# Performance work log

Hardware: AMD Instinct MI355X
Metric: run time of the kernel (lower is better)

The kernel has to match this reference:

```python
import jax, jax.numpy as jnp
import numpy as np

NUM_CODE = 8192
CODE_DIM = 256


def setup_inputs() -> dict:
    key = jax.random.key(0)
    k1, k2 = jax.random.split(key)
    z_e = jax.random.normal(k1, (16, CODE_DIM, 32, 32), dtype=jnp.float32)
    span = 1.0 / NUM_CODE
    codebook = jax.random.uniform(k2, (NUM_CODE, CODE_DIM), dtype=jnp.float32,
                                  minval=-span, maxval=span)
    return {"z_e": z_e, "codebook": codebook}


def reference(z_e, codebook):
    # NCHW -> NHWC
    z = jnp.transpose(z_e, (0, 2, 3, 1))  # [B,H,W,D]
    B, H, W, D = z.shape
    flat = z.reshape(-1, D)  # [N,D]
    cb = jax.lax.stop_gradient(codebook)
    # squared L2 distances without materializing [N,K,D] diff tensor
    z2 = jnp.sum(flat * flat, axis=1, keepdims=True)          # [N,1]
    c2 = jnp.sum(cb * cb, axis=1)                              # [K]
    dist = z2 - 2.0 * (flat @ cb.T) + c2[None, :]              # [N,K]
    indices = jnp.argmin(dist, axis=1)                         # [N]
    z_q_flat = cb[indices]                                     # [N,D]
    z_q = z_q_flat.reshape(B, H, W, D)
    # straight-through estimator
    z_q = z + jax.lax.stop_gradient(z_q - z)
    idx = indices.reshape(B, H, W)
    z_q = jnp.transpose(z_q, (0, 3, 1, 2))  # NHWC -> NCHW
    return z_q, idx
```

## Files before the change

kernel.cpp:

```cpp
#include <hip/hip_runtime.h>

typedef __attribute__((ext_vector_type(4))) unsigned int u32x4;
typedef __attribute__((ext_vector_type(4))) int i32x4;

union I16 { u32x4 u; i32x4 i; };

#define SA_INV   (127.0f / 12.0f)
#define SB_INV   (127.0f * 8192.0f)
#define INV_SASB ((127.0 * 127.0 * 8192.0) / 12.0)
#define WI       4500
#define FINF     3.4e38f

__device__ __forceinline__ int q8(float x, float s) {
    int q = (int)__builtin_rintf(x * s);
    return q < -127 ? -127 : (q > 127 ? 127 : q);
}
__device__ __forceinline__ unsigned int umin(unsigned int a, unsigned int b) { return a < b ? a : b; }
__device__ __forceinline__ unsigned int umax(unsigned int a, unsigned int b) { return a > b ? a : b; }

__global__ __launch_bounds__(256)
void prep_z(const float* __restrict__ z, u32x4* __restrict__ ahi,
            float* __restrict__ zt, float* __restrict__ z2f) {
    __shared__ float tile[32][257];
    __shared__ double pz[32][9];
    int bh = blockIdx.x;
    int b = bh >> 5, h = bh & 31;
    int tid = threadIdx.x;
    for (int e = tid; e < 8192; e += 256) {
        int d = e >> 5, w = e & 31;
        tile[w][d] = z[((size_t)(b * 256 + d) * 32 + h) * 32 + w];
    }
    __syncthreads();
    for (int e = tid; e < 8192; e += 256) {
        int w = e >> 8, d = e & 255;
        zt[(size_t)(bh * 32 + w) * 256 + d] = tile[w][d];
    }
    {
        int w = tid >> 3, seg = tid & 7;
        double s = 0.0;
#pragma unroll
        for (int d = 0; d < 32; ++d) { double v = (double)tile[w][seg * 32 + d]; s += v * v; }
        pz[w][seg] = s;
    }
    __syncthreads();
    if (tid < 32) {
        double s = 0.0;
#pragma unroll
        for (int seg = 0; seg < 8; ++seg) s += pz[tid][seg];
        z2f[bh * 32 + tid] = (float)s;
    }
    for (int o = tid; o < 512; o += 256) {
        int l = o & 63, j = (o >> 6) & 3, tt = o >> 8;
        int wp = tt * 16 + (l & 15);
        int k0 = j * 64 + ((l >> 4) << 4);
        u32x4 v;
#pragma unroll
        for (int d = 0; d < 4; ++d) {
            unsigned int wv = 0;
#pragma unroll
            for (int bb = 0; bb < 4; ++bb) {
                int q = q8(-2.0f * tile[wp][k0 + d * 4 + bb], SA_INV);
                wv |= ((unsigned int)(q & 255)) << (8 * bb);
            }
            v[d] = wv;
        }
        ahi[(size_t)bh * 512 + o] = v;
    }
}

__global__ __launch_bounds__(256)
void prep_cb(const float* __restrict__ cb, float* __restrict__ c2,
             unsigned int* __restrict__ ibt, u32x4* __restrict__ bstr) {
    __shared__ float tile[16][257];
    __shared__ float pc[16][17];
    int ct = blockIdx.x;
    int tid = threadIdx.x;
    int cl = tid >> 4, dseg = tid & 15;
    const float* src = cb + (size_t)(ct * 16 + cl) * 256 + dseg * 16;
    float s = 0.f;
#pragma unroll
    for (int i = 0; i < 16; ++i) { float v = src[i]; tile[cl][dseg * 16 + i] = v; s += v * v; }
    pc[cl][dseg] = s;
    __syncthreads();
    if (tid < 16) {
        float t = 0.f;
#pragma unroll
        for (int i = 0; i < 16; ++i) t += pc[tid][i];
        int code = ct * 16 + tid;
        c2[code] = t;
        int ib = (int)__builtin_rintf(t * (float)INV_SASB);
        ibt[code] = (((unsigned int)(ib + 262144)) << 6) | (unsigned int)((code >> 4) & 31);
    }
    int l = tid & 63, j = tid >> 6;
    int code_l = l & 15, k0 = j * 64 + ((l >> 4) << 4);
    u32x4 v;
#pragma unroll
    for (int d = 0; d < 4; ++d) {
        unsigned int wv = 0;
#pragma unroll
        for (int bb = 0; bb < 4; ++bb) {
            int q = q8(tile[code_l][k0 + d * 4 + bb], SB_INV);
            wv |= ((unsigned int)(q & 255)) << (8 * bb);
        }
        v[d] = wv;
    }
    bstr[(size_t)(ct * 4 + j) * 64 + l] = v;
}

__global__ __launch_bounds__(256)
void vq_main(const u32x4* __restrict__ ahi4, const u32x4* __restrict__ bstr,
             const unsigned int* __restrict__ ibt,
             unsigned int* __restrict__ cd, int* __restrict__ ci) {
    int tid = threadIdx.x;
    int wid = tid >> 6, lane = tid & 63;
    int stripe = blockIdx.x & 15;
    int rg = blockIdx.x >> 4;
    int colc = lane & 15;
    int rt0 = rg * 16 + wid * 4;

    I16 ah[4][4];
#pragma unroll
    for (int rt = 0; rt < 4; ++rt)
#pragma unroll
        for (int j = 0; j < 4; ++j)
            ah[rt][j].u = ahi4[((size_t)(rt0 + rt) * 4 + j) * 64 + lane];

    unsigned int m1[16], m2[16];
#pragma unroll
    for (int s = 0; s < 16; ++s) { m1[s] = 0xFFFFFFFFu; m2[s] = 0xFFFFFFFFu; }

    const u32x4* bbase = bstr + (size_t)stripe * 8192 + lane;
    const unsigned int* ibase = ibt + stripe * 512 + colc;
    i32x4 zc = (i32x4){0, 0, 0, 0};

    I16 bfA[4], bfB[4];
    unsigned int ibA, ibB;
#pragma unroll
    for (int j = 0; j < 4; ++j) bfA[j].u = bbase[j * 64];
    ibA = ibase[0];

    auto tilework = [&](const I16 (&bf)[4], unsigned int ibv) {
        i32x4 acc[4];
#pragma unroll
        for (int rt = 0; rt < 4; ++rt)
            acc[rt] = __builtin_amdgcn_mfma_i32_16x16x64_i8(ah[rt][0].i, bf[0].i, zc, 0, 0, 0);
#pragma unroll
        for (int j = 1; j < 4; ++j)
#pragma unroll
            for (int rt = 0; rt < 4; ++rt)
                acc[rt] = __builtin_amdgcn_mfma_i32_16x16x64_i8(ah[rt][j].i, bf[j].i, acc[rt], 0, 0, 0);
#pragma unroll
        for (int rt = 0; rt < 4; ++rt)
#pragma unroll
            for (int r = 0; r < 4; ++r) {
                unsigned int key = (((unsigned int)acc[rt][r]) << 6) + ibv;
                int s = rt * 4 + r;
                m2[s] = umin(umax(key, m1[s]), m2[s]);
                m1[s] = umin(m1[s], key);
            }
    };

    for (int t = 0; t < 32; t += 2) {
#pragma unroll
        for (int j = 0; j < 4; ++j) bfB[j].u = bbase[(t + 1) * 256 + j * 64];
        ibB = ibase[(t + 1) * 16];
        tilework(bfA, ibA);
        if (t + 2 < 32) {
#pragma unroll
            for (int j = 0; j < 4; ++j) bfA[j].u = bbase[(t + 2) * 256 + j * 64];
            ibA = ibase[(t + 2) * 16];
        }
        tilework(bfB, ibB);
    }

#pragma unroll
    for (int s = 0; s < 16; ++s) {
        int rt = s >> 2, r = s & 3;
        int row = (rt0 + rt) * 16 + (lane >> 4) * 4 + r;
        unsigned int v0 = m1[s], v1 = m2[s];
        int c0 = stripe * 512 + (int)(v0 & 63) * 16 + colc;
        int c1 = stripe * 512 + (int)(v1 & 63) * 16 + colc;
        int obase = (row * 16 + stripe) * 3;
#pragma unroll
        for (int k = 0; k < 3; ++k) {
            unsigned int bv; int bi;
            if (v1 < v0) { bv = v1; bi = c1; } else { bv = v0; bi = c0; }
#pragma unroll
            for (int mm = 1; mm < 16; mm <<= 1) {
                unsigned int ov = __shfl_xor(bv, mm, 64);
                int oi = __shfl_xor(bi, mm, 64);
                if (ov < bv || (ov == bv && oi < bi)) { bv = ov; bi = oi; }
            }
            if (colc == k) { cd[obase + k] = bv; ci[obase + k] = bi; }
            if (bi == c0) v0 = 0xFFFFFFFFu;
            if (bi == c1) v1 = 0xFFFFFFFFu;
        }
    }
}

__global__ __launch_bounds__(256)
void refine(const float* __restrict__ zt, const float* __restrict__ z2f,
            const float* __restrict__ cb, const float* __restrict__ c2,
            const unsigned int* __restrict__ cd, const int* __restrict__ ci,
            float* __restrict__ out, int* __restrict__ idxi) {
    int wid = threadIdx.x >> 6, lane = threadIdx.x & 63;
    int n = blockIdx.x * 4 + wid;
    float zq[4];
#pragma unroll
    for (int q = 0; q < 4; ++q) zq[q] = zt[(size_t)n * 256 + q * 64 + lane];
    float z2v = z2f[n];

    unsigned int kd = 0xFFFFFFFFu; int civ = 0;
    if (lane < 48) { kd = cd[n * 48 + lane]; civ = ci[n * 48 + lane]; }
    unsigned int rm = kd;
#pragma unroll
    for (int m = 32; m >= 1; m >>= 1) {
        unsigned int o = __shfl_xor(rm, m, 64);
        rm = o < rm ? o : rm;
    }
    bool active = (lane < 48) && ((kd >> 6) <= (rm >> 6) + WI);
    unsigned long long mask = __ballot(active);
    float bestd = FINF; int besti = 0x7fffffff;
    while (mask) {
        int k = __ffsll(mask) - 1;
        mask &= mask - 1;
        int cidx = __shfl(civ, k, 64);
        const float* crow = cb + (size_t)cidx * 256;
        double dot = 0.0;
#pragma unroll
        for (int q = 0; q < 4; ++q)
            dot += (double)zq[q] * (double)crow[q * 64 + lane];
#pragma unroll
        for (int m = 32; m >= 1; m >>= 1) dot += __shfl_xor(dot, m, 64);
        float Mf = (float)dot;
        float d1 = z2v - 2.0f * Mf;
        float d2 = d1 + c2[cidx];
        if (d2 < bestd || (d2 == bestd && cidx < besti)) { bestd = d2; besti = cidx; }
    }
    if (lane == 0) {
        idxi[n] = besti;
        out[4194304 + n] = (float)besti;
    }
}

__global__ void gather_out(const float* __restrict__ cb,
                           const int* __restrict__ idxi,
                           float* __restrict__ out) {
    __shared__ float tile[32][257];
    __shared__ int sidx[32];
    int b = blockIdx.x >> 5, h = blockIdx.x & 31;
    int tid = threadIdx.x;
    if (tid < 32) sidx[tid] = idxi[(b * 32 + h) * 32 + tid];
    __syncthreads();
    for (int e = tid; e < 8192; e += 256) {
        int w = e >> 8, d = e & 255;
        tile[w][d] = cb[(size_t)sidx[w] * 256 + d];
    }
    __syncthreads();
    for (int e = tid; e < 8192; e += 256) {
        int d = e >> 5, w = e & 31;
        out[(((size_t)b * 256 + d) * 32 + h) * 32 + w] = tile[w][d];
    }
}

extern "C" void kernel_launch(void* const* d_in, const int* in_sizes, int n_in,
                              void* d_out, int out_size, void* d_ws, size_t ws_size,
                              hipStream_t stream) {
    const float* z  = (const float*)d_in[0];
    const float* cb = (const float*)d_in[1];
    float* out = (float*)d_out;
    char* w = (char*)d_ws;
    u32x4* ahi  = (u32x4*)(w);
    u32x4* bstr = (u32x4*)(w + 4194304);
    float* zt   = (float*)(w + 6291456);
    float* c2   = (float*)(w + 23068672);
    unsigned int* ibt = (unsigned int*)(w + 23101440);
    float* z2f  = (float*)(w + 23134208);
    unsigned int* cd = (unsigned int*)(w + 23199744);
    int*   ci   = (int*)(w + 26345472);
    int*   idxi = (int*)(w);

    prep_cb<<<512, 256, 0, stream>>>(cb, c2, ibt, bstr);
    prep_z<<<512, 256, 0, stream>>>(z, ahi, zt, z2f);
    vq_main<<<1024, 256, 0, stream>>>(ahi, bstr, ibt, cd, ci);
    refine<<<4096, 256, 0, stream>>>(zt, z2f, cb, c2, cd, ci, out, idxi);
    gather_out<<<512, 256, 0, stream>>>(cb, idxi, out);
}
```

Before: 179.6 us.

## Halve per-wave row tiles in vq_main, double grid, inline-asm top-2 update

Each wave of vq_main now covers 2 row tiles instead of 4, so the A-fragment and top-2 state registers are halved and the grid doubles to 2048 blocks. This lowers register pressure to allow more resident waves and better latency hiding. The top-2 min update is written as inline asm using v_lshl_add_u32/max/min, and the B pointers are advanced incrementally instead of recomputed. In exchange, each B tile loaded from memory is reused across fewer rows, which doubles codebook traffic per row.

Result: faster. 164.7 us (-8.3%).

```diff
diff --git a/kernel.cpp b/kernel.cpp
--- a/kernel.cpp
+++ b/kernel.cpp
@@ -15,8 +15,6 @@
     int q = (int)__builtin_rintf(x * s);
     return q < -127 ? -127 : (q > 127 ? 127 : q);
 }
-__device__ __forceinline__ unsigned int umin(unsigned int a, unsigned int b) { return a < b ? a : b; }
-__device__ __forceinline__ unsigned int umax(unsigned int a, unsigned int b) { return a > b ? a : b; }
 
 __global__ __launch_bounds__(256)
 void prep_z(const float* __restrict__ z, u32x4* __restrict__ ahi,
@@ -116,65 +114,69 @@
     int stripe = blockIdx.x & 15;
     int rg = blockIdx.x >> 4;
     int colc = lane & 15;
-    int rt0 = rg * 16 + wid * 4;
-
-    I16 ah[4][4];
-#pragma unroll
-    for (int rt = 0; rt < 4; ++rt)
+    int rt0 = rg * 8 + wid * 2;
+
+    I16 ah[2][4];
+#pragma unroll
+    for (int rt = 0; rt < 2; ++rt)
 #pragma unroll
         for (int j = 0; j < 4; ++j)
             ah[rt][j].u = ahi4[((size_t)(rt0 + rt) * 4 + j) * 64 + lane];
 
-    unsigned int m1[16], m2[16];
-#pragma unroll
-    for (int s = 0; s < 16; ++s) { m1[s] = 0xFFFFFFFFu; m2[s] = 0xFFFFFFFFu; }
-
-    const u32x4* bbase = bstr + (size_t)stripe * 8192 + lane;
-    const unsigned int* ibase = ibt + stripe * 512 + colc;
+    unsigned int m1[8], m2[8];
+#pragma unroll
+    for (int s = 0; s < 8; ++s) { m1[s] = 0xFFFFFFFFu; m2[s] = 0xFFFFFFFFu; }
+
+    const u32x4* p0 = bstr + (size_t)stripe * 8192 + lane;
+    const u32x4* p1 = p0 + 256;
+    const unsigned int* ip = ibt + stripe * 512 + colc;
     i32x4 zc = (i32x4){0, 0, 0, 0};
 
     I16 bfA[4], bfB[4];
     unsigned int ibA, ibB;
 #pragma unroll
-    for (int j = 0; j < 4; ++j) bfA[j].u = bbase[j * 64];
-    ibA = ibase[0];
+    for (int j = 0; j < 4; ++j) bfA[j].u = p0[j * 64];
+    ibA = ip[0];
 
     auto tilework = [&](const I16 (&bf)[4], unsigned int ibv) {
-        i32x4 acc[4];
-#pragma unroll
-        for (int rt = 0; rt < 4; ++rt)
-            acc[rt] = __builtin_amdgcn_mfma_i32_16x16x64_i8(ah[rt][0].i, bf[0].i, zc, 0, 0, 0);
-#pragma unroll
-        for (int j = 1; j < 4; ++j)
-#pragma unroll
-            for (int rt = 0; rt < 4; ++rt)
-                acc[rt] = __builtin_amdgcn_mfma_i32_16x16x64_i8(ah[rt][j].i, bf[j].i, acc[rt], 0, 0, 0);
-#pragma unroll
-        for (int rt = 0; rt < 4; ++rt)
-#pragma unroll
-            for (int r = 0; r < 4; ++r) {
-                unsigned int key = (((unsigned int)acc[rt][r]) << 6) + ibv;
-                int s = rt * 4 + r;
-                m2[s] = umin(umax(key, m1[s]), m2[s]);
-                m1[s] = umin(m1[s], key);
-            }
+        i32x4 acc0, acc1;
+        acc0 = __builtin_amdgcn_mfma_i32_16x16x64_i8(ah[0][0].i, bf[0].i, zc, 0, 0, 0);
+        acc1 = __builtin_amdgcn_mfma_i32_16x16x64_i8(ah[1][0].i, bf[0].i, zc, 0, 0, 0);
+#pragma unroll
+        for (int j = 1; j < 4; ++j) {
+            acc0 = __builtin_amdgcn_mfma_i32_16x16x64_i8(ah[0][j].i, bf[j].i, acc0, 0, 0, 0);
+            acc1 = __builtin_amdgcn_mfma_i32_16x16x64_i8(ah[1][j].i, bf[j].i, acc1, 0, 0, 0);
+        }
+#pragma unroll
+        for (int s = 0; s < 8; ++s) {
+            unsigned int av = (unsigned int)((s < 4) ? acc0[s & 3] : acc1[s & 3]);
+            unsigned int key, tmp;
+            asm("v_lshl_add_u32 %0, %4, 6, %5\n\t"
+                "v_max_u32 %1, %0, %2\n\t"
+                "v_min_u32 %3, %3, %1\n\t"
+                "v_min_u32 %2, %2, %0"
+                : "=&v"(key), "=&v"(tmp), "+v"(m1[s]), "+v"(m2[s])
+                : "v"(av), "v"(ibv));
+        }
     };
 
     for (int t = 0; t < 32; t += 2) {
 #pragma unroll
-        for (int j = 0; j < 4; ++j) bfB[j].u = bbase[(t + 1) * 256 + j * 64];
-        ibB = ibase[(t + 1) * 16];
+        for (int j = 0; j < 4; ++j) bfB[j].u = p1[j * 64];
+        ibB = ip[(t + 1) * 16];
         tilework(bfA, ibA);
         if (t + 2 < 32) {
-#pragma unroll
-            for (int j = 0; j < 4; ++j) bfA[j].u = bbase[(t + 2) * 256 + j * 64];
-            ibA = ibase[(t + 2) * 16];
+            p0 += 512;
+#pragma unroll
+            for (int j = 0; j < 4; ++j) bfA[j].u = p0[j * 64];
+            ibA = ip[(t + 2) * 16];
         }
         tilework(bfB, ibB);
-    }
-
-#pragma unroll
-    for (int s = 0; s < 16; ++s) {
+        p1 += 512;
+    }
+
+#pragma unroll
+    for (int s = 0; s < 8; ++s) {
         int rt = s >> 2, r = s & 3;
         int row = (rt0 + rt) * 16 + (lane >> 4) * 4 + r;
         unsigned int v0 = m1[s], v1 = m2[s];
@@ -282,7 +284,7 @@
 
     prep_cb<<<512, 256, 0, stream>>>(cb, c2, ibt, bstr);
     prep_z<<<512, 256, 0, stream>>>(z, ahi, zt, z2f);
-    vq_main<<<1024, 256, 0, stream>>>(ahi, bstr, ibt, cd, ci);
+    vq_main<<<2048, 256, 0, stream>>>(ahi, bstr, ibt, cd, ci);
     refine<<<4096, 256, 0, stream>>>(zt, z2f, cb, c2, cd, ci, out, idxi);
     gather_out<<<512, 256, 0, stream>>>(cb, idxi, out);
 }
```
